# Performance work log

Measured on AMD Instinct MI355X. Metric: run time of the kernel, lower is better.

## Reference

```python
import jax, jax.numpy as jnp
import numpy as np

N = 50000
E = 800000
IN_C = 512
HID = 256
NUM_CLASS = (10, 25, 16, 350)


def _glorot(key, shape):
    fan_in, fan_out = shape[0], shape[1]
    lim = float(np.sqrt(6.0 / (fan_in + fan_out)))
    return jax.random.uniform(key, shape, jnp.float32, -lim, lim)


def setup_inputs() -> dict:
    key = jax.random.key(0)
    ks = jax.random.split(key, 16)
    x = jax.random.normal(ks[0], (N, IN_C), jnp.float32)
    edge_index = jax.random.randint(ks[1], (2, E), 0, N, jnp.int32)
    inp = {"x": x, "edge_index": edge_index}
    # gc1
    inp["W1"] = _glorot(ks[2], (IN_C, HID)); inp["b1"] = jnp.zeros((HID,), jnp.float32)
    # four GCNConv heads
    names = ["type", "school", "time", "author"]
    for i, (nm, nc) in enumerate(zip(names, NUM_CLASS)):
        inp[f"Wg_{nm}"] = _glorot(ks[3 + i], (HID, nc))
        inp[f"bg_{nm}"] = jnp.zeros((nc,), jnp.float32)
        inp[f"Wc_{nm}"] = _glorot(ks[7 + i], (nc, nc))
        inp[f"bc_{nm}"] = jnp.zeros((nc,), jnp.float32)
    return inp


def gcn_conv(x, W, b, src, dst, n):
    # GCNConv: out = D^{-1/2} (A + I) D^{-1/2} (x W) + b, symmetric norm.
    xw = x @ W  # [N, out]
    ones = jnp.ones((src.shape[0],), xw.dtype)
    deg = jax.ops.segment_sum(ones, dst, num_segments=n) + 1.0  # +1 from self-loop
    dinv = jax.lax.rsqrt(deg)
    norm = dinv[src] * dinv[dst]  # [E]
    agg = jax.ops.segment_sum(xw[src] * norm[:, None], dst, num_segments=n)
    # self-loop contribution: norm_ii = dinv_i^2
    return agg + xw * (dinv * dinv)[:, None] + b


def reference(x, edge_index, W1, b1,
              Wg_type, bg_type, Wc_type, bc_type,
              Wg_school, bg_school, Wc_school, bc_school,
              Wg_time, bg_time, Wc_time, bc_time,
              Wg_author, bg_author, Wc_author, bc_author):
    src, dst = edge_index[0], edge_index[1]
    n = x.shape[0]
    h = jax.nn.relu(gcn_conv(x, W1, b1, src, dst, n))  # dropout is identity in eval

    def head(Wg, bg, Wc, bc):
        g = gcn_conv(h, Wg, bg, src, dst, n)
        return jax.nn.softmax(g @ Wc + bc, axis=-1)

    out_type = head(Wg_type, bg_type, Wc_type, bc_type)
    out_school = head(Wg_school, bg_school, Wc_school, bc_school)
    out_time = head(Wg_time, bg_time, Wc_time, bc_time)
    out_author = head(Wg_author, bg_author, Wc_author, bc_author)
    return (out_type, out_school, out_time, out_author)
```

## Files before the change

kernel.cpp:

```cpp
#include <hip/hip_runtime.h>
#include <hip/hip_bf16.h>
#include <cstdint>
#include <cstddef>
#include <math.h>

#define NN 50000
#define NE 800000
#define INC 512
#define HIDC 256
#define NBLK ((NN + 255) / 256)

typedef __attribute__((ext_vector_type(8))) short s8v;
typedef __attribute__((ext_vector_type(4))) float f4v;

__device__ __forceinline__ float b2f(unsigned short u) {
    return __uint_as_float(((unsigned)u) << 16);
}
__device__ __forceinline__ unsigned short f2b(float f) {
    __hip_bfloat16 h = __float2bfloat16(f);
    return *reinterpret_cast<unsigned short*>(&h);
}

__global__ void k_zero_i(int* a, int n) {
    int i = blockIdx.x * 256 + threadIdx.x;
    if (i < n) a[i] = 0;
}
__global__ void k_deg_count(const int* __restrict__ dst, int* __restrict__ cnt, int e) {
    int i = blockIdx.x * 256 + threadIdx.x;
    if (i < e) atomicAdd(&cnt[dst[i]], 1);
}
__global__ void k_dinv(const int* __restrict__ cnt, float* __restrict__ dinv, int n) {
    int i = blockIdx.x * 256 + threadIdx.x;
    if (i < n) dinv[i] = rsqrtf((float)cnt[i] + 1.0f);
}
__global__ void k_scan1(const int* __restrict__ cnt, int* __restrict__ excl,
                        int* __restrict__ bsum, int n) {
    __shared__ int s[256];
    int i = blockIdx.x * 256 + threadIdx.x;
    int v = (i < n) ? cnt[i] : 0;
    s[threadIdx.x] = v;
    __syncthreads();
    for (int off = 1; off < 256; off <<= 1) {
        int t = (threadIdx.x >= off) ? s[threadIdx.x - off] : 0;
        __syncthreads();
        s[threadIdx.x] += t;
        __syncthreads();
    }
    if (i < n) excl[i] = s[threadIdx.x] - v;
    if (threadIdx.x == 255) bsum[blockIdx.x] = s[255];
}
__global__ void k_scan2(int* __restrict__ bsum, int* __restrict__ bsumx, int nb) {
    __shared__ int s[256];
    int t = threadIdx.x;
    int v = (t < nb) ? bsum[t] : 0;
    s[t] = v;
    __syncthreads();
    for (int off = 1; off < 256; off <<= 1) {
        int tt = (t >= off) ? s[t - off] : 0;
        __syncthreads();
        s[t] += tt;
        __syncthreads();
    }
    if (t < nb) bsumx[t] = s[t] - v;
}
__global__ void k_scan3(int* __restrict__ rowptr, const int* __restrict__ bsumx, int n, int e) {
    int i = blockIdx.x * 256 + threadIdx.x;
    if (i < n) rowptr[i] += bsumx[blockIdx.x];
    if (i == 0) rowptr[n] = e;
}
__global__ void k_fill(const int* __restrict__ src, const int* __restrict__ dst,
                       const int* __restrict__ rowptr, int* __restrict__ cursor,
                       int* __restrict__ col, int e) {
    int i = blockIdx.x * 256 + threadIdx.x;
    if (i >= e) return;
    int d = dst[i];
    int pos = rowptr[d] + atomicAdd(&cursor[d], 1);
    col[pos] = src[i];
}

__global__ void k_packW1t(const float* __restrict__ W1, unsigned short* __restrict__ W1t) {
    int t = blockIdx.x * 256 + threadIdx.x;
    if (t >= 256 * 512) return;
    int c = t >> 9, k = t & 511;
    W1t[t] = f2b(W1[(size_t)k * 256 + c]);
}
__global__ void k_tr(const float* __restrict__ W, float* __restrict__ Wt, int nc) {
    int t = blockIdx.x * 256 + threadIdx.x;
    if (t >= 256 * nc) return;
    int k = t / nc, i = t - k * nc;
    Wt[i * 256 + k] = W[t];
}
__global__ void k_fold(const float* __restrict__ Wgt3, const float* __restrict__ Wc3,
                       const float* __restrict__ Wgt0, const float* __restrict__ Wc0,
                       const float* __restrict__ Wgt1, const float* __restrict__ Wc1,
                       const float* __restrict__ Wgt2, const float* __restrict__ Wc2,
                       unsigned short* __restrict__ Wft) {
    int t = blockIdx.x * 256 + threadIdx.x;
    if (t >= 448 * 256) return;
    int j = t >> 8, k = t & 255;
    float s = 0.f;
    if (j < 350)              { for (int i = 0; i < 350; ++i) s += Wgt3[i * 256 + k] * Wc3[(size_t)i * 350 + j]; }
    else if (j >= 352 && j < 362) { int jj = j - 352; for (int i = 0; i < 10; ++i) s += Wgt0[i * 256 + k] * Wc0[i * 10 + jj]; }
    else if (j >= 362 && j < 387) { int jj = j - 362; for (int i = 0; i < 25; ++i) s += Wgt1[i * 256 + k] * Wc1[i * 25 + jj]; }
    else if (j >= 387 && j < 403) { int jj = j - 387; for (int i = 0; i < 16; ++i) s += Wgt2[i * 256 + k] * Wc2[i * 16 + jj]; }
    Wft[t] = f2b(s);
}
__global__ void k_foldb(const float* __restrict__ bg3, const float* __restrict__ bc3, const float* __restrict__ Wc3,
                        const float* __restrict__ bg0, const float* __restrict__ bc0, const float* __restrict__ Wc0,
                        const float* __restrict__ bg1, const float* __restrict__ bc1, const float* __restrict__ Wc1,
                        const float* __restrict__ bg2, const float* __restrict__ bc2, const float* __restrict__ Wc2,
                        float* __restrict__ bfv) {
    int j = blockIdx.x * 64 + threadIdx.x;
    if (j >= 448) return;
    float s = 0.f;
    if (j < 350)              { s = bc3[j]; for (int i = 0; i < 350; ++i) s += bg3[i] * Wc3[(size_t)i * 350 + j]; }
    else if (j >= 352 && j < 362) { int jj = j - 352; s = bc0[jj]; for (int i = 0; i < 10; ++i) s += bg0[i] * Wc0[i * 10 + jj]; }
    else if (j >= 362 && j < 387) { int jj = j - 362; s = bc1[jj]; for (int i = 0; i < 25; ++i) s += bg1[i] * Wc1[i * 25 + jj]; }
    else if (j >= 387 && j < 403) { int jj = j - 387; s = bc2[jj]; for (int i = 0; i < 16; ++i) s += bg2[i] * Wc2[i * 16 + jj]; }
    bfv[j] = s;
}

__global__ __launch_bounds__(256) void gemm1_conv(
    const float* __restrict__ X, const unsigned short* __restrict__ Bt,
    unsigned short* __restrict__ C, int M)
{
    __shared__ s8v As[512];
    __shared__ s8v Bs[2048];
    const int t = threadIdx.x;
    const int lane = t & 63, wv = t >> 6;
    const int row0 = blockIdx.x * 64;
    const int l15 = lane & 15, lq = lane >> 4, l7 = lane & 7;

    f4v acc[16] = {};
    for (int k0 = 0; k0 < 512; k0 += 64) {
#pragma unroll
        for (int s = 0; s < 2; ++s) {
            int c = s * 256 + t;
            int row = c >> 3, ch = c & 7;
            int chg = ch ^ (row & 7);
            int gr = row0 + row; if (gr >= M) gr = M - 1;
            const float* src = X + (size_t)gr * 512 + k0 + chg * 8;
            float4 a = *(const float4*)src;
            float4 b = *(const float4*)(src + 4);
            s8v o;
            o[0] = (short)f2b(a.x); o[1] = (short)f2b(a.y);
            o[2] = (short)f2b(a.z); o[3] = (short)f2b(a.w);
            o[4] = (short)f2b(b.x); o[5] = (short)f2b(b.y);
            o[6] = (short)f2b(b.z); o[7] = (short)f2b(b.w);
            As[c] = o;
        }
#pragma unroll
        for (int s = 0; s < 8; ++s) {
            int c = s * 256 + t;
            int colr = c >> 3, ch = c & 7;
            int chg = ch ^ (colr & 7);
            Bs[c] = *(const s8v*)(Bt + (size_t)colr * 512 + k0 + chg * 8);
        }
        __syncthreads();
#pragma unroll
        for (int kk = 0; kk < 2; ++kk) {
            s8v af = As[(wv * 16 + l15) * 8 + ((kk * 4 + lq) ^ l7)];
#pragma unroll
            for (int cf = 0; cf < 16; ++cf) {
                s8v bfr = Bs[(cf * 16 + l15) * 8 + ((kk * 4 + lq) ^ l7)];
                acc[cf] = __builtin_amdgcn_mfma_f32_16x16x32_bf16(af, bfr, acc[cf], 0, 0, 0);
            }
        }
        __syncthreads();
    }
#pragma unroll
    for (int cf = 0; cf < 16; ++cf)
#pragma unroll
        for (int r = 0; r < 4; ++r) {
            int row = row0 + wv * 16 + lq * 4 + r;
            if (row < M) C[(size_t)row * 256 + cf * 16 + l15] = f2b(acc[cf][r]);
        }
}

template <bool RELU, bool BIAS>
__global__ __launch_bounds__(256) void k_gather2(
    const unsigned short* __restrict__ feat, const int* __restrict__ rowptr,
    const int* __restrict__ col, const float* __restrict__ dinv,
    const float* __restrict__ bias, unsigned short* __restrict__ out, int n)
{
    int unit = (blockIdx.x * 256 + threadIdx.x) >> 5;
    int l32 = threadIdx.x & 31;
    if (unit >= n) return;
    float di = dinv[unit];
    int p0 = rowptr[unit], p1 = rowptr[unit + 1];
    int deg = p1 - p0;
    int myc = 0; float mydj = 0.f;
    if (l32 < deg) { myc = col[p0 + l32]; mydj = dinv[myc]; }
    float acc[8] = {};
    int dmin = deg < 32 ? deg : 32;
    int base = threadIdx.x & 32;
#pragma unroll 2
    for (int q = 0; q < dmin; ++q) {
        int j = __shfl(myc, base + q);
        float dj = __shfl(mydj, base + q);
        s8v v = *(const s8v*)(feat + (size_t)j * HIDC + l32 * 8);
#pragma unroll
        for (int c = 0; c < 8; ++c) acc[c] += dj * b2f((unsigned short)v[c]);
    }
    for (int p = p0 + 32; p < p1; ++p) {
        int j = col[p];
        float dj = dinv[j];
        s8v v = *(const s8v*)(feat + (size_t)j * HIDC + l32 * 8);
#pragma unroll
        for (int c = 0; c < 8; ++c) acc[c] += dj * b2f((unsigned short)v[c]);
    }
    s8v sv = *(const s8v*)(feat + (size_t)unit * HIDC + l32 * 8);
    float dd = di * di;
    s8v o;
#pragma unroll
    for (int c = 0; c < 8; ++c) {
        float r = di * acc[c] + dd * b2f((unsigned short)sv[c]);
        if (BIAS) r += bias[l32 * 8 + c];
        if (RELU) r = fmaxf(r, 0.f);
        o[c] = (short)f2b(r);
    }
    *(s8v*)(out + (size_t)unit * HIDC + l32 * 8) = o;
}

__global__ __launch_bounds__(256) void gemm2_heads(
    const unsigned short* __restrict__ A, const unsigned short* __restrict__ Bt,
    const float* __restrict__ bfv,
    float* __restrict__ o0, float* __restrict__ o1,
    float* __restrict__ o2, float* __restrict__ o3, int M)
{
    __shared__ s8v As[512];
    __shared__ s8v Bs[3584];
    const int t = threadIdx.x;
    const int lane = t & 63, wv = t >> 6;
    const int row0 = blockIdx.x * 64;
    const int l15 = lane & 15, lq = lane >> 4, l7 = lane & 7;

    f4v acc[28] = {};
    for (int k0 = 0; k0 < 256; k0 += 64) {
#pragma unroll
        for (int s = 0; s < 2; ++s) {
            int c = s * 256 + t;
            int row = c >> 3, ch = c & 7;
            int chg = ch ^ (row & 7);
            int gr = row0 + row; if (gr >= M) gr = M - 1;
            As[c] = *(const s8v*)(A + (size_t)gr * 256 + k0 + chg * 8);
        }
#pragma unroll
        for (int s = 0; s < 14; ++s) {
            int c = s * 256 + t;
            int colr = c >> 3, ch = c & 7;
            int chg = ch ^ (colr & 7);
            Bs[c] = *(const s8v*)(Bt + (size_t)colr * 256 + k0 + chg * 8);
        }
        __syncthreads();
#pragma unroll
        for (int kk = 0; kk < 2; ++kk) {
            s8v af = As[(wv * 16 + l15) * 8 + ((kk * 4 + lq) ^ l7)];
#pragma unroll
            for (int cf = 0; cf < 28; ++cf) {
                s8v bfr = Bs[(cf * 16 + l15) * 8 + ((kk * 4 + lq) ^ l7)];
                acc[cf] = __builtin_amdgcn_mfma_f32_16x16x32_bf16(af, bfr, acc[cf], 0, 0, 0);
            }
        }
        __syncthreads();
    }
#pragma unroll
    for (int cf = 0; cf < 28; ++cf) {
        float b = bfv[cf * 16 + l15];
#pragma unroll
        for (int r = 0; r < 4; ++r) acc[cf][r] += b;
    }
#pragma unroll
    for (int r = 0; r < 4; ++r) {
        int row = row0 + wv * 16 + lq * 4 + r;
        float m0 = -1e30f, m1 = -1e30f, m2 = -1e30f, m3 = -1e30f;
#pragma unroll
        for (int cf = 0; cf < 28; ++cf) {
            int colc = cf * 16 + l15;
            float xv = acc[cf][r];
            if (colc < 350) m0 = fmaxf(m0, xv);
            else if (colc >= 352 && colc < 362) m1 = fmaxf(m1, xv);
            else if (colc >= 362 && colc < 387) m2 = fmaxf(m2, xv);
            else if (colc >= 387 && colc < 403) m3 = fmaxf(m3, xv);
        }
#pragma unroll
        for (int o = 8; o; o >>= 1) {
            m0 = fmaxf(m0, __shfl_xor(m0, o));
            m1 = fmaxf(m1, __shfl_xor(m1, o));
            m2 = fmaxf(m2, __shfl_xor(m2, o));
            m3 = fmaxf(m3, __shfl_xor(m3, o));
        }
        float s0 = 0.f, s1 = 0.f, s2 = 0.f, s3 = 0.f;
#pragma unroll
        for (int cf = 0; cf < 28; ++cf) {
            int colc = cf * 16 + l15;
            float xv = acc[cf][r];
            float e = 0.f;
            if (colc < 350)                     { e = __expf(xv - m0); s0 += e; }
            else if (colc >= 352 && colc < 362) { e = __expf(xv - m1); s1 += e; }
            else if (colc >= 362 && colc < 387) { e = __expf(xv - m2); s2 += e; }
            else if (colc >= 387 && colc < 403) { e = __expf(xv - m3); s3 += e; }
            acc[cf][r] = e;
        }
#pragma unroll
        for (int o = 8; o; o >>= 1) {
            s0 += __shfl_xor(s0, o); s1 += __shfl_xor(s1, o);
            s2 += __shfl_xor(s2, o); s3 += __shfl_xor(s3, o);
        }
        float i0 = 1.f / s0, i1 = 1.f / s1, i2 = 1.f / s2, i3 = 1.f / s3;
        if (row < M) {
#pragma unroll
            for (int cf = 0; cf < 28; ++cf) {
                int colc = cf * 16 + l15;
                float e = acc[cf][r];
                if (colc < 350)                     o3[(size_t)row * 350 + colc]       = e * i0;
                else if (colc >= 352 && colc < 362) o0[(size_t)row * 10 + colc - 352]  = e * i1;
                else if (colc >= 362 && colc < 387) o1[(size_t)row * 25 + colc - 362]  = e * i2;
                else if (colc >= 387 && colc < 403) o2[(size_t)row * 16 + colc - 387]  = e * i3;
            }
        }
    }
}

extern "C" void kernel_launch(void* const* d_in, const int* in_sizes, int n_in,
                              void* d_out, int out_size, void* d_ws, size_t ws_size,
                              hipStream_t stream)
{
    const float* x   = (const float*)d_in[0];
    const int*   ei  = (const int*)d_in[1];
    const float* W1  = (const float*)d_in[2];
    const float* b1  = (const float*)d_in[3];
    const float* Wg0 = (const float*)d_in[4];
    const float* bg0 = (const float*)d_in[5];
    const float* Wc0 = (const float*)d_in[6];
    const float* bc0 = (const float*)d_in[7];
    const float* Wg1 = (const float*)d_in[8];
    const float* bg1 = (const float*)d_in[9];
    const float* Wc1 = (const float*)d_in[10];
    const float* bc1 = (const float*)d_in[11];
    const float* Wg2 = (const float*)d_in[12];
    const float* bg2 = (const float*)d_in[13];
    const float* Wc2 = (const float*)d_in[14];
    const float* bc2 = (const float*)d_in[15];
    const float* Wg3 = (const float*)d_in[16];
    const float* bg3 = (const float*)d_in[17];
    const float* Wc3 = (const float*)d_in[18];
    const float* bc3 = (const float*)d_in[19];
    const int* srcI = ei;
    const int* dstI = ei + NE;

    char* ws = (char*)d_ws;
    size_t off = 0;
    auto alloc = [&](size_t bytes) { void* p = ws + off; off += (bytes + 255) & ~(size_t)255; return p; };
    float* dinv   = (float*)alloc(50176 * 4);
    int*   rowptr = (int*)  alloc(50432 * 4);
    int*   cnt    = (int*)  alloc(2 * 50176 * 4);
    int*   cursor = cnt + 50176;
    int*   bsum   = (int*)  alloc(1024);
    int*   bsumx  = (int*)  alloc(1024);
    int*   col    = (int*)  alloc((size_t)NE * 4);
    unsigned short* W1t = (unsigned short*)alloc(256 * 512 * 2);
    unsigned short* Wft = (unsigned short*)alloc(448 * 256 * 2);
    float* bfv   = (float*)alloc(448 * 4);
    float* Wgt3  = (float*)alloc(350 * 256 * 4);
    float* Wgt0  = (float*)alloc(10 * 256 * 4);
    float* Wgt1  = (float*)alloc(25 * 256 * 4);
    float* Wgt2  = (float*)alloc(16 * 256 * 4);
    unsigned short* xwb = (unsigned short*)alloc((size_t)NN * HIDC * 2);
    unsigned short* hb  = (unsigned short*)alloc((size_t)NN * HIDC * 2);
    unsigned short* ahb = xwb;

    float* out0 = (float*)d_out;
    float* out1 = out0 + (size_t)NN * 10;
    float* out2 = out1 + (size_t)NN * 25;
    float* out3 = out2 + (size_t)NN * 16;

    k_zero_i<<<(2 * 50176 + 255) / 256, 256, 0, stream>>>(cnt, 2 * 50176);
    k_deg_count<<<(NE + 255) / 256, 256, 0, stream>>>(dstI, cnt, NE);
    k_dinv<<<NBLK, 256, 0, stream>>>(cnt, dinv, NN);
    k_scan1<<<NBLK, 256, 0, stream>>>(cnt, rowptr, bsum, NN);
    k_scan2<<<1, 256, 0, stream>>>(bsum, bsumx, NBLK);
    k_scan3<<<NBLK, 256, 0, stream>>>(rowptr, bsumx, NN, NE);
    k_fill<<<(NE + 255) / 256, 256, 0, stream>>>(srcI, dstI, rowptr, cursor, col, NE);

    k_packW1t<<<(256 * 512 + 255) / 256, 256, 0, stream>>>(W1, W1t);
    k_tr<<<350, 256, 0, stream>>>(Wg3, Wgt3, 350);
    k_tr<<<10, 256, 0, stream>>>(Wg0, Wgt0, 10);
    k_tr<<<25, 256, 0, stream>>>(Wg1, Wgt1, 25);
    k_tr<<<16, 256, 0, stream>>>(Wg2, Wgt2, 16);
    k_fold<<<448, 256, 0, stream>>>(Wgt3, Wc3, Wgt0, Wc0, Wgt1, Wc1, Wgt2, Wc2, Wft);
    k_foldb<<<7, 64, 0, stream>>>(bg3, bc3, Wc3, bg0, bc0, Wc0, bg1, bc1, Wc1, bg2, bc2, Wc2, bfv);

    gemm1_conv<<<(NN + 63) / 64, 256, 0, stream>>>(x, W1t, xwb, NN);
    k_gather2<true, true><<<(NN + 7) / 8, 256, 0, stream>>>(xwb, rowptr, col, dinv, b1, hb, NN);
    k_gather2<false, false><<<(NN + 7) / 8, 256, 0, stream>>>(hb, rowptr, col, dinv, nullptr, ahb, NN);
    gemm2_heads<<<(NN + 63) / 64, 256, 0, stream>>>(ahb, Wft, bfv, out0, out1, out2, out3, NN);
}
```

Measured before the change: 357.5 us.

## Merge prep kernels, fold dinv into scan, and shrink GEMM K-tiles with padded LDS

Replaces the zero kernel with hipMemsetAsync and computes dinv inside the first scan kernel. Merges the W1 pack, head-weight transposes, fold and bias-fold kernels into one k_prep launch that reads Wg directly, removing the intermediate transposed buffers. Both GEMMs move from 64-wide K tiles with XOR-swizzled LDS to 32-wide K tiles with a padded stride of 5, using less shared memory but needing twice as many sync iterations. The main aim is fewer kernel launches; the GEMM change trades barrier count and load width for smaller LDS and simpler indexing.

```diff
diff --git a/kernel.cpp b/kernel.cpp
--- a/kernel.cpp
+++ b/kernel.cpp
@@ -21,23 +21,16 @@
     return *reinterpret_cast<unsigned short*>(&h);
 }
 
-__global__ void k_zero_i(int* a, int n) {
-    int i = blockIdx.x * 256 + threadIdx.x;
-    if (i < n) a[i] = 0;
-}
 __global__ void k_deg_count(const int* __restrict__ dst, int* __restrict__ cnt, int e) {
     int i = blockIdx.x * 256 + threadIdx.x;
     if (i < e) atomicAdd(&cnt[dst[i]], 1);
 }
-__global__ void k_dinv(const int* __restrict__ cnt, float* __restrict__ dinv, int n) {
-    int i = blockIdx.x * 256 + threadIdx.x;
-    if (i < n) dinv[i] = rsqrtf((float)cnt[i] + 1.0f);
-}
 __global__ void k_scan1(const int* __restrict__ cnt, int* __restrict__ excl,
-                        int* __restrict__ bsum, int n) {
+                        int* __restrict__ bsum, float* __restrict__ dinv, int n) {
     __shared__ int s[256];
     int i = blockIdx.x * 256 + threadIdx.x;
     int v = (i < n) ? cnt[i] : 0;
+    if (i < n) dinv[i] = rsqrtf((float)v + 1.0f);
     s[threadIdx.x] = v;
     __syncthreads();
     for (int off = 1; off < 256; off <<= 1) {
@@ -78,93 +71,82 @@
     col[pos] = src[i];
 }
 
-__global__ void k_packW1t(const float* __restrict__ W1, unsigned short* __restrict__ W1t) {
-    int t = blockIdx.x * 256 + threadIdx.x;
-    if (t >= 256 * 512) return;
-    int c = t >> 9, k = t & 511;
-    W1t[t] = f2b(W1[(size_t)k * 256 + c]);
-}
-__global__ void k_tr(const float* __restrict__ W, float* __restrict__ Wt, int nc) {
-    int t = blockIdx.x * 256 + threadIdx.x;
-    if (t >= 256 * nc) return;
-    int k = t / nc, i = t - k * nc;
-    Wt[i * 256 + k] = W[t];
-}
-__global__ void k_fold(const float* __restrict__ Wgt3, const float* __restrict__ Wc3,
-                       const float* __restrict__ Wgt0, const float* __restrict__ Wc0,
-                       const float* __restrict__ Wgt1, const float* __restrict__ Wc1,
-                       const float* __restrict__ Wgt2, const float* __restrict__ Wc2,
-                       unsigned short* __restrict__ Wft) {
-    int t = blockIdx.x * 256 + threadIdx.x;
-    if (t >= 448 * 256) return;
-    int j = t >> 8, k = t & 255;
-    float s = 0.f;
-    if (j < 350)              { for (int i = 0; i < 350; ++i) s += Wgt3[i * 256 + k] * Wc3[(size_t)i * 350 + j]; }
-    else if (j >= 352 && j < 362) { int jj = j - 352; for (int i = 0; i < 10; ++i) s += Wgt0[i * 256 + k] * Wc0[i * 10 + jj]; }
-    else if (j >= 362 && j < 387) { int jj = j - 362; for (int i = 0; i < 25; ++i) s += Wgt1[i * 256 + k] * Wc1[i * 25 + jj]; }
-    else if (j >= 387 && j < 403) { int jj = j - 387; for (int i = 0; i < 16; ++i) s += Wgt2[i * 256 + k] * Wc2[i * 16 + jj]; }
-    Wft[t] = f2b(s);
-}
-__global__ void k_foldb(const float* __restrict__ bg3, const float* __restrict__ bc3, const float* __restrict__ Wc3,
-                        const float* __restrict__ bg0, const float* __restrict__ bc0, const float* __restrict__ Wc0,
-                        const float* __restrict__ bg1, const float* __restrict__ bc1, const float* __restrict__ Wc1,
-                        const float* __restrict__ bg2, const float* __restrict__ bc2, const float* __restrict__ Wc2,
-                        float* __restrict__ bfv) {
-    int j = blockIdx.x * 64 + threadIdx.x;
-    if (j >= 448) return;
-    float s = 0.f;
-    if (j < 350)              { s = bc3[j]; for (int i = 0; i < 350; ++i) s += bg3[i] * Wc3[(size_t)i * 350 + j]; }
-    else if (j >= 352 && j < 362) { int jj = j - 352; s = bc0[jj]; for (int i = 0; i < 10; ++i) s += bg0[i] * Wc0[i * 10 + jj]; }
-    else if (j >= 362 && j < 387) { int jj = j - 362; s = bc1[jj]; for (int i = 0; i < 25; ++i) s += bg1[i] * Wc1[i * 25 + jj]; }
-    else if (j >= 387 && j < 403) { int jj = j - 387; s = bc2[jj]; for (int i = 0; i < 16; ++i) s += bg2[i] * Wc2[i * 16 + jj]; }
-    bfv[j] = s;
+__global__ void k_prep(const float* __restrict__ W1,
+                       const float* __restrict__ Wg0, const float* __restrict__ Wc0,
+                       const float* __restrict__ bg0, const float* __restrict__ bc0,
+                       const float* __restrict__ Wg1, const float* __restrict__ Wc1,
+                       const float* __restrict__ bg1, const float* __restrict__ bc1,
+                       const float* __restrict__ Wg2, const float* __restrict__ Wc2,
+                       const float* __restrict__ bg2, const float* __restrict__ bc2,
+                       const float* __restrict__ Wg3, const float* __restrict__ Wc3,
+                       const float* __restrict__ bg3, const float* __restrict__ bc3,
+                       unsigned short* __restrict__ W1t, unsigned short* __restrict__ Wft,
+                       float* __restrict__ bfv)
+{
+    int b = blockIdx.x, tid = threadIdx.x;
+    if (b < 512) {
+        int t = b * 256 + tid;
+        int c = t >> 9, k = t & 511;
+        W1t[t] = f2b(W1[(size_t)k * 256 + c]);
+    } else if (b < 960) {
+        int j = b - 512, k = tid;
+        float s = 0.f;
+        if (j < 350)                  { for (int i = 0; i < 350; ++i) s += Wg3[k * 350 + i] * Wc3[(size_t)i * 350 + j]; }
+        else if (j >= 352 && j < 362) { int jj = j - 352; for (int i = 0; i < 10; ++i) s += Wg0[k * 10 + i] * Wc0[i * 10 + jj]; }
+        else if (j >= 362 && j < 387) { int jj = j - 362; for (int i = 0; i < 25; ++i) s += Wg1[k * 25 + i] * Wc1[i * 25 + jj]; }
+        else if (j >= 387 && j < 403) { int jj = j - 387; for (int i = 0; i < 16; ++i) s += Wg2[k * 16 + i] * Wc2[i * 16 + jj]; }
+        Wft[j * 256 + k] = f2b(s);
+    } else {
+        int j = (b - 960) * 256 + tid;
+        if (j >= 448) return;
+        float s = 0.f;
+        if (j < 350)                  { s = bc3[j]; for (int i = 0; i < 350; ++i) s += bg3[i] * Wc3[(size_t)i * 350 + j]; }
+        else if (j >= 352 && j < 362) { int jj = j - 352; s = bc0[jj]; for (int i = 0; i < 10; ++i) s += bg0[i] * Wc0[i * 10 + jj]; }
+        else if (j >= 362 && j < 387) { int jj = j - 362; s = bc1[jj]; for (int i = 0; i < 25; ++i) s += bg1[i] * Wc1[i * 25 + jj]; }
+        else if (j >= 387 && j < 403) { int jj = j - 387; s = bc2[jj]; for (int i = 0; i < 16; ++i) s += bg2[i] * Wc2[i * 16 + jj]; }
+        bfv[j] = s;
+    }
 }
 
 __global__ __launch_bounds__(256) void gemm1_conv(
     const float* __restrict__ X, const unsigned short* __restrict__ Bt,
     unsigned short* __restrict__ C, int M)
 {
-    __shared__ s8v As[512];
-    __shared__ s8v Bs[2048];
+    __shared__ s8v As[64 * 5];
+    __shared__ s8v Bs[256 * 5];
     const int t = threadIdx.x;
     const int lane = t & 63, wv = t >> 6;
     const int row0 = blockIdx.x * 64;
-    const int l15 = lane & 15, lq = lane >> 4, l7 = lane & 7;
+    const int l15 = lane & 15, lq = lane >> 4;
+
+    const int arow = t >> 2, ach = t & 3;
+    int gr = row0 + arow; if (gr >= M) gr = M - 1;
+    const float* asrc = X + (size_t)gr * 512 + ach * 8;
 
     f4v acc[16] = {};
-    for (int k0 = 0; k0 < 512; k0 += 64) {
-#pragma unroll
-        for (int s = 0; s < 2; ++s) {
-            int c = s * 256 + t;
-            int row = c >> 3, ch = c & 7;
-            int chg = ch ^ (row & 7);
-            int gr = row0 + row; if (gr >= M) gr = M - 1;
-            const float* src = X + (size_t)gr * 512 + k0 + chg * 8;
-            float4 a = *(const float4*)src;
-            float4 b = *(const float4*)(src + 4);
+    for (int k0 = 0; k0 < 512; k0 += 32) {
+        {
+            float4 a = *(const float4*)(asrc + k0);
+            float4 b = *(const float4*)(asrc + k0 + 4);
             s8v o;
             o[0] = (short)f2b(a.x); o[1] = (short)f2b(a.y);
             o[2] = (short)f2b(a.z); o[3] = (short)f2b(a.w);
             o[4] = (short)f2b(b.x); o[5] = (short)f2b(b.y);
             o[6] = (short)f2b(b.z); o[7] = (short)f2b(b.w);
-            As[c] = o;
-        }
-#pragma unroll
-        for (int s = 0; s < 8; ++s) {
+            As[arow * 5 + ach] = o;
+        }
+#pragma unroll
+        for (int s = 0; s < 4; ++s) {
             int c = s * 256 + t;
-            int colr = c >> 3, ch = c & 7;
-            int chg = ch ^ (colr & 7);
-            Bs[c] = *(const s8v*)(Bt + (size_t)colr * 512 + k0 + chg * 8);
-        }
-        __syncthreads();
-#pragma unroll
-        for (int kk = 0; kk < 2; ++kk) {
-            s8v af = As[(wv * 16 + l15) * 8 + ((kk * 4 + lq) ^ l7)];
-#pragma unroll
-            for (int cf = 0; cf < 16; ++cf) {
-                s8v bfr = Bs[(cf * 16 + l15) * 8 + ((kk * 4 + lq) ^ l7)];
-                acc[cf] = __builtin_amdgcn_mfma_f32_16x16x32_bf16(af, bfr, acc[cf], 0, 0, 0);
-            }
+            int colr = c >> 2, ch = c & 3;
+            Bs[colr * 5 + ch] = *(const s8v*)(Bt + (size_t)colr * 512 + k0 + ch * 8);
+        }
+        __syncthreads();
+        s8v af = As[(wv * 16 + l15) * 5 + lq];
+#pragma unroll
+        for (int cf = 0; cf < 16; ++cf) {
+            s8v bfr = Bs[(cf * 16 + l15) * 5 + lq];
+            acc[cf] = __builtin_amdgcn_mfma_f32_16x16x32_bf16(af, bfr, acc[cf], 0, 0, 0);
         }
         __syncthreads();
     }
@@ -228,39 +210,32 @@
     float* __restrict__ o0, float* __restrict__ o1,
     float* __restrict__ o2, float* __restrict__ o3, int M)
 {
-    __shared__ s8v As[512];
-    __shared__ s8v Bs[3584];
+    __shared__ s8v As[64 * 5];
+    __shared__ s8v Bs[448 * 5];
     const int t = threadIdx.x;
     const int lane = t & 63, wv = t >> 6;
     const int row0 = blockIdx.x * 64;
-    const int l15 = lane & 15, lq = lane >> 4, l7 = lane & 7;
+    const int l15 = lane & 15, lq = lane >> 4;
+
+    const int arow = t >> 2, ach = t & 3;
+    int gr = row0 + arow; if (gr >= M) gr = M - 1;
+    const unsigned short* asrc = A + (size_t)gr * 256 + ach * 8;
 
     f4v acc[28] = {};
-    for (int k0 = 0; k0 < 256; k0 += 64) {
-#pragma unroll
-        for (int s = 0; s < 2; ++s) {
+    for (int k0 = 0; k0 < 256; k0 += 32) {
+        As[arow * 5 + ach] = *(const s8v*)(asrc + k0);
+#pragma unroll
+        for (int s = 0; s < 7; ++s) {
             int c = s * 256 + t;
-            int row = c >> 3, ch = c & 7;
-            int chg = ch ^ (row & 7);
-            int gr = row0 + row; if (gr >= M) gr = M - 1;
-            As[c] = *(const s8v*)(A + (size_t)gr * 256 + k0 + chg * 8);
-        }
-#pragma unroll
-        for (int s = 0; s < 14; ++s) {
-            int c = s * 256 + t;
-            int colr = c >> 3, ch = c & 7;
-            int chg = ch ^ (colr & 7);
-            Bs[c] = *(const s8v*)(Bt + (size_t)colr * 256 + k0 + chg * 8);
-        }
-        __syncthreads();
-#pragma unroll
-        for (int kk = 0; kk < 2; ++kk) {
-            s8v af = As[(wv * 16 + l15) * 8 + ((kk * 4 + lq) ^ l7)];
-#pragma unroll
-            for (int cf = 0; cf < 28; ++cf) {
-                s8v bfr = Bs[(cf * 16 + l15) * 8 + ((kk * 4 + lq) ^ l7)];
-                acc[cf] = __builtin_amdgcn_mfma_f32_16x16x32_bf16(af, bfr, acc[cf], 0, 0, 0);
-            }
+            int colr = c >> 2, ch = c & 3;
+            Bs[colr * 5 + ch] = *(const s8v*)(Bt + (size_t)colr * 256 + k0 + ch * 8);
+        }
+        __syncthreads();
+        s8v af = As[(wv * 16 + l15) * 5 + lq];
+#pragma unroll
+        for (int cf = 0; cf < 28; ++cf) {
+            s8v bfr = Bs[(cf * 16 + l15) * 5 + lq];
+            acc[cf] = __builtin_amdgcn_mfma_f32_16x16x32_bf16(af, bfr, acc[cf], 0, 0, 0);
         }
         __syncthreads();
     }
@@ -362,10 +337,6 @@
     unsigned short* W1t = (unsigned short*)alloc(256 * 512 * 2);
     unsigned short* Wft = (unsigned short*)alloc(448 * 256 * 2);
     float* bfv   = (float*)alloc(448 * 4);
-    float* Wgt3  = (float*)alloc(350 * 256 * 4);
-    float* Wgt0  = (float*)alloc(10 * 256 * 4);
-    float* Wgt1  = (float*)alloc(25 * 256 * 4);
-    float* Wgt2  = (float*)alloc(16 * 256 * 4);
     unsigned short* xwb = (unsigned short*)alloc((size_t)NN * HIDC * 2);
     unsigned short* hb  = (unsigned short*)alloc((size_t)NN * HIDC * 2);
     unsigned short* ahb = xwb;
@@ -375,21 +346,17 @@
     float* out2 = out1 + (size_t)NN * 25;
     float* out3 = out2 + (size_t)NN * 16;
 
-    k_zero_i<<<(2 * 50176 + 255) / 256, 256, 0, stream>>>(cnt, 2 * 50176);
+    hipMemsetAsync(cnt, 0, 2 * 50176 * 4, stream);
     k_deg_count<<<(NE + 255) / 256, 256, 0, stream>>>(dstI, cnt, NE);
-    k_dinv<<<NBLK, 256, 0, stream>>>(cnt, dinv, NN);
-    k_scan1<<<NBLK, 256, 0, stream>>>(cnt, rowptr, bsum, NN);
+    k_scan1<<<NBLK, 256, 0, stream>>>(cnt, rowptr, bsum, dinv, NN);
     k_scan2<<<1, 256, 0, stream>>>(bsum, bsumx, NBLK);
     k_scan3<<<NBLK, 256, 0, stream>>>(rowptr, bsumx, NN, NE);
     k_fill<<<(NE + 255) / 256, 256, 0, stream>>>(srcI, dstI, rowptr, cursor, col, NE);
 
-    k_packW1t<<<(256 * 512 + 255) / 256, 256, 0, stream>>>(W1, W1t);
-    k_tr<<<350, 256, 0, stream>>>(Wg3, Wgt3, 350);
-    k_tr<<<10, 256, 0, stream>>>(Wg0, Wgt0, 10);
-    k_tr<<<25, 256, 0, stream>>>(Wg1, Wgt1, 25);
-    k_tr<<<16, 256, 0, stream>>>(Wg2, Wgt2, 16);
-    k_fold<<<448, 256, 0, stream>>>(Wgt3, Wc3, Wgt0, Wc0, Wgt1, Wc1, Wgt2, Wc2, Wft);
-    k_foldb<<<7, 64, 0, stream>>>(bg3, bc3, Wc3, bg0, bc0, Wc0, bg1, bc1, Wc1, bg2, bc2, Wc2, bfv);
+    k_prep<<<962, 256, 0, stream>>>(W1,
+                                    Wg0, Wc0, bg0, bc0, Wg1, Wc1, bg1, bc1,
+                                    Wg2, Wc2, bg2, bc2, Wg3, Wc3, bg3, bc3,
+                                    W1t, Wft, bfv);
 
     gemm1_conv<<<(NN + 63) / 64, 256, 0, stream>>>(x, W1t, xwb, NN);
     k_gather2<true, true><<<(NN + 7) / 8, 256, 0, stream>>>(xwb, rowptr, col, dinv, b1, hb, NN);
```

Measured after the change: 328.0 us. -8.2%, faster.
